# Kernel tuning notes

Hardware: AMD Instinct MI355X
Metric: run time of the kernel (lower is better)

The kernel has to match this reference:

```python
import jax, jax.numpy as jnp
import numpy as np

HEADS = 8
DIM_HEAD = 64
SCALE = DIM_HEAD ** -0.5
EPS = 1e-5


def layernorm(t, g, b):
    mu = t.mean(-1, keepdims=True)
    var = ((t - mu) ** 2).mean(-1, keepdims=True)
    return (t - mu) * jax.lax.rsqrt(var + EPS) * g + b


def setup_inputs() -> dict:
    key = jax.random.key(0)
    ks = jax.random.split(key, 12)
    b, n, dim, inner = 2, 2048, 512, HEADS * DIM_HEAD
    s = dim ** -0.5
    return {
        "x": jax.random.normal(ks[0], (b, n, dim), jnp.float32),
        "context": jax.random.normal(ks[1], (b, n, dim), jnp.float32),
        "g_x": jnp.ones((dim,), jnp.float32),
        "b_x": jnp.zeros((dim,), jnp.float32),
        "g_c": jnp.ones((dim,), jnp.float32),
        "b_c": jnp.zeros((dim,), jnp.float32),
        "W_qk": jax.random.normal(ks[2], (dim, inner), jnp.float32) * s,
        "W_cqk": jax.random.normal(ks[3], (dim, inner), jnp.float32) * s,
        "W_v": jax.random.normal(ks[4], (dim, inner), jnp.float32) * s,
        "W_cv": jax.random.normal(ks[5], (dim, inner), jnp.float32) * s,
        "W_out": jax.random.normal(ks[6], (inner, dim), jnp.float32) * s,
        "b_out": jnp.zeros((dim,), jnp.float32),
        "W_cout": jax.random.normal(ks[7], (inner, dim), jnp.float32) * s,
        "b_cout": jnp.zeros((dim,), jnp.float32),
    }


def reference(x, context, g_x, b_x, g_c, b_c, W_qk, W_cqk, W_v, W_cv, W_out, b_out, W_cout, b_cout):
    b, i, _ = x.shape
    j = context.shape[1]
    xn = layernorm(x, g_x, b_x)
    cn = layernorm(context, g_c, b_c)

    def split_heads(t):  # [b, n, h*d] -> [b, h, n, d]
        return t.reshape(t.shape[0], t.shape[1], HEADS, DIM_HEAD).transpose(0, 2, 1, 3)

    qk = split_heads(xn @ W_qk)
    cqk = split_heads(cn @ W_cqk)
    v = split_heads(xn @ W_v)
    cv = split_heads(cn @ W_cv)

    sim = jnp.einsum('bhid,bhjd->bhij', qk, cqk) * SCALE  # [b,h,i,j]
    attn = jax.nn.softmax(sim, axis=-1)           # rows: x attends to context
    context_attn = jax.nn.softmax(sim, axis=-2)   # cols: context attends to x

    out = jnp.einsum('bhij,bhjd->bhid', attn, cv)            # [b,h,i,d]
    context_out = jnp.einsum('bhij,bhid->bhjd', context_attn, v)  # [b,h,j,d]

    def merge_heads(t):  # [b,h,n,d] -> [b,n,h*d]
        return t.transpose(0, 2, 1, 3).reshape(t.shape[0], t.shape[2], HEADS * DIM_HEAD)

    out = merge_heads(out) @ W_out + b_out
    context_out = merge_heads(context_out) @ W_cout + b_cout
    return out, context_out
```

## Files before the change

### kernel.cpp

```cpp
#include <hip/hip_runtime.h>


typedef _Float16 half_t;
typedef __attribute__((ext_vector_type(2))) _Float16 half2v;
typedef __attribute__((ext_vector_type(4))) _Float16 half4v;
typedef __attribute__((ext_vector_type(8))) _Float16 half8v;
typedef __attribute__((ext_vector_type(4))) float floatx4;

#define MFMA16(a, b, c) __builtin_amdgcn_mfma_f32_16x16x32_f16((a), (b), (c), 0, 0, 0)

#if defined(__has_builtin)
#if __has_builtin(__builtin_amdgcn_exp2f)
#define EXP2F(x) __builtin_amdgcn_exp2f(x)
#else
#define EXP2F(x) exp2f(x)
#endif
#else
#define EXP2F(x) exp2f(x)
#endif

__device__ __forceinline__ half2v pk2(float a, float b) {
#if defined(__has_builtin) && __has_builtin(__builtin_amdgcn_cvt_pkrtz)
    union { __fp16 __attribute__((ext_vector_type(2))) i; half2v o; } u;
    u.i = __builtin_amdgcn_cvt_pkrtz(a, b);
    return u.o;
#else
    half2v r; r[0] = (half_t)a; r[1] = (half_t)b; return r;
#endif
}

__device__ __forceinline__ void gld16(const half_t* g, half_t* l) {
    __builtin_amdgcn_global_load_lds(
        (const __attribute__((address_space(1))) void*)g,
        (__attribute__((address_space(3))) void*)l, 16, 0, 0);
}

__global__ __launch_bounds__(256) void prep_kernel(
    const float* __restrict__ x, const float* __restrict__ ctx,
    const float* __restrict__ gx, const float* __restrict__ bx,
    const float* __restrict__ gc, const float* __restrict__ bc,
    half_t* __restrict__ xn, half_t* __restrict__ cn,
    const float* __restrict__ W0, const float* __restrict__ W1,
    const float* __restrict__ W2, const float* __restrict__ W3,
    const float* __restrict__ W4, const float* __restrict__ W5,
    half_t* __restrict__ Wt)
{
    __shared__ alignas(16) half_t Ts[128][136];
    const int blk = blockIdx.x;
    const int tid = threadIdx.x;
    const int wave = tid >> 6, lane = tid & 63;

    if (blk < 2048) {
        const int row = blk * 4 + wave;
        const float *src, *g, *b;
        half_t* dst;
        if (row < 4096) {
            src = x + (size_t)row * 512; g = gx; b = bx; dst = xn + (size_t)row * 512;
        } else {
            const size_t r = (size_t)(row - 4096);
            src = ctx + r * 512; g = gc; b = bc; dst = cn + r * 512;
        }
        const float4 a0 = *(const float4*)(src + lane * 4);
        const float4 a1 = *(const float4*)(src + 256 + lane * 4);
        float s = a0.x + a0.y + a0.z + a0.w + a1.x + a1.y + a1.z + a1.w;
        float q = a0.x * a0.x + a0.y * a0.y + a0.z * a0.z + a0.w * a0.w +
                  a1.x * a1.x + a1.y * a1.y + a1.z * a1.z + a1.w * a1.w;
#pragma unroll
        for (int m = 1; m < 64; m <<= 1) {
            s += __shfl_xor(s, m);
            q += __shfl_xor(q, m);
        }
        const float mean = s * (1.0f / 512.0f);
        const float var = q * (1.0f / 512.0f) - mean * mean;
        const float rs = rsqrtf(var + 1e-5f);
        const float4 g0 = *(const float4*)(g + lane * 4);
        const float4 g1 = *(const float4*)(g + 256 + lane * 4);
        const float4 b0 = *(const float4*)(b + lane * 4);
        const float4 b1 = *(const float4*)(b + 256 + lane * 4);
        half4v h0, h1;
        h0[0] = (half_t)((a0.x - mean) * rs * g0.x + b0.x);
        h0[1] = (half_t)((a0.y - mean) * rs * g0.y + b0.y);
        h0[2] = (half_t)((a0.z - mean) * rs * g0.z + b0.z);
        h0[3] = (half_t)((a0.w - mean) * rs * g0.w + b0.w);
        h1[0] = (half_t)((a1.x - mean) * rs * g1.x + b1.x);
        h1[1] = (half_t)((a1.y - mean) * rs * g1.y + b1.y);
        h1[2] = (half_t)((a1.z - mean) * rs * g1.z + b1.z);
        h1[3] = (half_t)((a1.w - mean) * rs * g1.w + b1.w);
        *(half4v*)(dst + lane * 4) = h0;
        *(half4v*)(dst + 256 + lane * 4) = h1;
        return;
    }

    const int b2 = blk - 2048;
    const int mat = b2 >> 4, tile = b2 & 15;
    const float* src;
    switch (mat) {
        case 0: src = W0; break;
        case 1: src = W1; break;
        case 2: src = W2; break;
        case 3: src = W3; break;
        case 4: src = W4; break;
        default: src = W5; break;
    }
    const int tr0 = (tile >> 2) * 128;
    const int tc0 = (tile & 3) * 128;
#pragma unroll
    for (int p = 0; p < 16; ++p) {
        const int idx = p * 256 + tid;
        const int r = idx >> 5, c4 = (idx & 31) * 4;
        const float4 w = *(const float4*)(src + (size_t)(tr0 + r) * 512 + tc0 + c4);
        Ts[c4 + 0][r] = (half_t)w.x;
        Ts[c4 + 1][r] = (half_t)w.y;
        Ts[c4 + 2][r] = (half_t)w.z;
        Ts[c4 + 3][r] = (half_t)w.w;
    }
    __syncthreads();
    half_t* dst = Wt + (size_t)mat * 262144;
#pragma unroll
    for (int p = 0; p < 8; ++p) {
        const int idx = p * 256 + tid;
        const int row = idx >> 4, ch = (idx & 15) * 8;
        *(half8v*)(dst + (size_t)(tc0 + row) * 512 + tr0 + ch) = *(const half8v*)&Ts[row][ch];
    }
}

__global__ __launch_bounds__(256) void gemm_in_kernel(
    const half_t* __restrict__ xn, const half_t* __restrict__ cn,
    const half_t* __restrict__ Wt,
    half_t* __restrict__ qk, half_t* __restrict__ v_t,
    half_t* __restrict__ cqk, half_t* __restrict__ cv_t)
{
    const half_t* A; const half_t* B; half_t* O;
    switch (blockIdx.z) {
        case 0:  A = xn; B = Wt;          O = qk;   break;
        case 1:  A = xn; B = Wt + 262144; O = v_t;  break;
        case 2:  A = cn; B = Wt + 524288; O = cqk;  break;
        default: A = cn; B = Wt + 786432; O = cv_t; break;
    }
    const int tr = blockIdx.z & 1;
    const int mt0 = blockIdx.x * 128;
    const int nt0 = blockIdx.y * 128;

    __shared__ alignas(16) half_t As[128 * 64];
    __shared__ alignas(16) half_t Ws[128 * 64];

    const int tid = threadIdx.x;
    const int wave = tid >> 6, lane = tid & 63;
    const int wr = wave >> 1, wc = wave & 1;
    const int q4 = lane >> 4, c = lane & 15;

    int srow[4], scol[4];
#pragma unroll
    for (int p = 0; p < 4; ++p) {
        const int ofs = p * 4096 + wave * 1024 + lane * 16;
        const int row = ofs >> 7;
        const int pc = (ofs >> 4) & 7;
        srow[p] = row;
        scol[p] = (pc ^ (row & 7)) * 8;
    }

    const half_t* P1 = tr ? As : Ws;
    const half_t* P2 = tr ? Ws : As;

    const floatx4 z4 = {0.f, 0.f, 0.f, 0.f};
    floatx4 acc[4][4];
#pragma unroll
    for (int mt = 0; mt < 4; ++mt)
#pragma unroll
        for (int nt = 0; nt < 4; ++nt) acc[mt][nt] = z4;

    for (int kb = 0; kb < 8; ++kb) {
        const int k0 = kb * 64;
#pragma unroll
        for (int p = 0; p < 4; ++p) {
            const int lofs = p * 2048 + wave * 512;
            gld16(A + (size_t)(mt0 + srow[p]) * 512 + k0 + scol[p], As + lofs);
            gld16(B + (size_t)(nt0 + srow[p]) * 512 + k0 + scol[p], Ws + lofs);
        }
        __syncthreads();
#pragma unroll
        for (int kt = 0; kt < 2; ++kt) {
            half8v f1[4], f2[4];
#pragma unroll
            for (int i = 0; i < 4; ++i) {
                const int r1 = wr * 64 + i * 16 + c;
                const int r2 = wc * 64 + i * 16 + c;
                f1[i] = *(const half8v*)&P1[(r1 << 6) + (((kt * 4 + q4) ^ (r1 & 7)) << 3)];
                f2[i] = *(const half8v*)&P2[(r2 << 6) + (((kt * 4 + q4) ^ (r2 & 7)) << 3)];
            }
#pragma unroll
            for (int mt = 0; mt < 4; ++mt)
#pragma unroll
                for (int nt = 0; nt < 4; ++nt)
                    acc[mt][nt] = MFMA16(f1[mt], f2[nt], acc[mt][nt]);
        }
        __syncthreads();
    }

    const int bb = mt0 >> 11;
    const int nnb = mt0 & 2047;
    if (tr) {
#pragma unroll
        for (int mt = 0; mt < 4; ++mt) {
            const int row = nnb + wr * 64 + mt * 16 + q4 * 4;
#pragma unroll
            for (int nt = 0; nt < 4; ++nt) {
                const int col = nt0 + wc * 64 + nt * 16 + c;
                const int h = col >> 6, dd = col & 63;
                half4v pk;
                pk[0] = (half_t)acc[mt][nt][0];
                pk[1] = (half_t)acc[mt][nt][1];
                pk[2] = (half_t)acc[mt][nt][2];
                pk[3] = (half_t)acc[mt][nt][3];
                *(half4v*)(O + ((size_t)(bb * 8 + h) * 64 + dd) * 2048 + row) = pk;
            }
        }
    } else {
#pragma unroll
        for (int mt = 0; mt < 4; ++mt) {
            const int colw = nt0 + wr * 64 + mt * 16 + q4 * 4;
            const int h = colw >> 6, dd = colw & 63;
#pragma unroll
            for (int nt = 0; nt < 4; ++nt) {
                const int row = nnb + wc * 64 + nt * 16 + c;
                half4v pk;
                pk[0] = (half_t)acc[mt][nt][0];
                pk[1] = (half_t)acc[mt][nt][1];
                pk[2] = (half_t)acc[mt][nt][2];
                pk[3] = (half_t)acc[mt][nt][3];
                *(half4v*)(O + ((size_t)(bb * 8 + h) * 2048 + row) * 64 + dd) = pk;
            }
        }
    }
}

__global__ __launch_bounds__(256, 2) void flash_kernel(
    const half_t* __restrict__ qk, const half_t* __restrict__ cqk,
    const half_t* __restrict__ v_t, const half_t* __restrict__ cv_t,
    half_t* __restrict__ out_h, half_t* __restrict__ ctx_out_h)
{
    const int bh = blockIdx.x, it = blockIdx.y, dir = blockIdx.z;
    const half_t* Q  = dir ? cqk : qk;
    const half_t* K  = dir ? qk  : cqk;
    const half_t* VT = dir ? v_t : cv_t;
    half_t* Out = dir ? ctx_out_h : out_h;
    const half_t* Qb = Q + (size_t)bh * (2048 * 64);
    const half_t* Kb = K + (size_t)bh * (2048 * 64);
    const half_t* VTb = VT + (size_t)bh * (64 * 2048);

    __shared__ alignas(16) half_t Ks[128 * 64];
    __shared__ alignas(16) half_t CVs[64 * 128];

    const int tid = threadIdx.x;
    const int wave = tid >> 6, lane = tid & 63;
    const int q4 = lane >> 4, c = lane & 15;

    half8v onesb;
#pragma unroll
    for (int j = 0; j < 8; ++j) onesb[j] = (c == 0) ? (half_t)1.0f : (half_t)0.0f;

    half8v qf[2][2];
#pragma unroll
    for (int mt = 0; mt < 2; ++mt)
#pragma unroll
        for (int kt = 0; kt < 2; ++kt) {
            half8v v = *(const half8v*)(Qb + (size_t)(it * 128 + wave * 32 + mt * 16 + c) * 64 +
                                        kt * 32 + q4 * 8);
            qf[mt][kt] = v * (half_t)0.18033688f;
        }

    const floatx4 z4 = {0.f, 0.f, 0.f, 0.f};
    floatx4 accT[4][2];
    floatx4 accL[2];
#pragma unroll
    for (int vt = 0; vt < 4; ++vt)
#pragma unroll
        for (int mt = 0; mt < 2; ++mt) accT[vt][mt] = z4;
    accL[0] = z4; accL[1] = z4;

    half8v kpre[4], vpre[4];
#pragma unroll
    for (int p = 0; p < 4; ++p) {
        const int cidx = p * 256 + tid;
        kpre[p] = *(const half8v*)(Kb + (size_t)(cidx >> 3) * 64 + (cidx & 7) * 8);
        vpre[p] = *(const half8v*)(VTb + (size_t)(cidx >> 4) * 2048 + (cidx & 15) * 8);
    }

    for (int jt = 0; jt < 16; ++jt) {
        __syncthreads();
#pragma unroll
        for (int p = 0; p < 4; ++p) {
            const int cidx = p * 256 + tid;
            const int krow = cidx >> 3, kch = cidx & 7;
            *(half8v*)&Ks[krow * 64 + ((kch ^ ((krow >> 2) & 7)) * 8)] = kpre[p];
            const int vrow = cidx >> 4, vch = cidx & 15;
            *(half8v*)&CVs[vrow * 128 + ((vch ^ (vrow & 15)) * 8)] = vpre[p];
        }
        __syncthreads();
        if (jt < 15) {
            const half_t* Kt = Kb + (size_t)(jt + 1) * 8192;
            const half_t* Vt = VTb + (jt + 1) * 128;
#pragma unroll
            for (int p = 0; p < 4; ++p) {
                const int cidx = p * 256 + tid;
                kpre[p] = *(const half8v*)(Kt + (size_t)(cidx >> 3) * 64 + (cidx & 7) * 8);
                vpre[p] = *(const half8v*)(Vt + (size_t)(cidx >> 4) * 2048 + (cidx & 15) * 8);
            }
        }

#pragma unroll
        for (int g = 0; g < 4; ++g) {
            floatx4 st[2][2];
#pragma unroll
            for (int t = 0; t < 2; ++t) {
                const int jr = g * 32 + t * 4 + ((c >> 2) << 3) + (c & 3);
                const int sw = (jr >> 2) & 7;
                const half8v kf0 = *(const half8v*)&Ks[jr * 64 + ((q4 ^ sw) * 8)];
                const half8v kf1 = *(const half8v*)&Ks[jr * 64 + (((4 + q4) ^ sw) * 8)];
#pragma unroll
                for (int mt = 0; mt < 2; ++mt) {
                    floatx4 tt = MFMA16(kf0, qf[mt][0], z4);
                    st[mt][t] = MFMA16(kf1, qf[mt][1], tt);
                }
            }
            half8v pf[2];
#pragma unroll
            for (int mt = 0; mt < 2; ++mt) {
                union { half8v v; half2v h2[4]; } u;
                u.h2[0] = pk2(EXP2F(fminf(st[mt][0][0], 15.0f)),
                              EXP2F(fminf(st[mt][0][1], 15.0f)));
                u.h2[1] = pk2(EXP2F(fminf(st[mt][0][2], 15.0f)),
                              EXP2F(fminf(st[mt][0][3], 15.0f)));
                u.h2[2] = pk2(EXP2F(fminf(st[mt][1][0], 15.0f)),
                              EXP2F(fminf(st[mt][1][1], 15.0f)));
                u.h2[3] = pk2(EXP2F(fminf(st[mt][1][2], 15.0f)),
                              EXP2F(fminf(st[mt][1][3], 15.0f)));
                pf[mt] = u.v;
            }
#pragma unroll
            for (int vt = 0; vt < 4; ++vt) {
                const half8v bf = *(const half8v*)&CVs[(vt * 16 + c) * 128 +
                                                       (((g * 4 + q4) ^ c) * 8)];
#pragma unroll
                for (int mt = 0; mt < 2; ++mt)
                    accT[vt][mt] = MFMA16(bf, pf[mt], accT[vt][mt]);
            }
#pragma unroll
            for (int mt = 0; mt < 2; ++mt)
                accL[mt] = MFMA16(onesb, pf[mt], accL[mt]);
        }
    }

    const size_t ob = (size_t)(bh >> 3) * 2048 * 512 + (size_t)(bh & 7) * 64;
#pragma unroll
    for (int mt = 0; mt < 2; ++mt) {
        const float l = __shfl(accL[mt][0], c);
        const float rl = 1.0f / l;
        const int row = it * 128 + wave * 32 + mt * 16 + c;
#pragma unroll
        for (int vt = 0; vt < 4; ++vt) {
            half4v pk;
            pk[0] = (half_t)(accT[vt][mt][0] * rl);
            pk[1] = (half_t)(accT[vt][mt][1] * rl);
            pk[2] = (half_t)(accT[vt][mt][2] * rl);
            pk[3] = (half_t)(accT[vt][mt][3] * rl);
            *(half4v*)(Out + ob + (size_t)row * 512 + vt * 16 + q4 * 4) = pk;
        }
    }
}

__global__ __launch_bounds__(256) void gemm_out_kernel(
    const half_t* __restrict__ out_h, const half_t* __restrict__ ctx_out_h,
    const half_t* __restrict__ Wt,
    const float* __restrict__ bout, const float* __restrict__ bcout,
    float* __restrict__ dout)
{
    const half_t* A; const half_t* B; const float* bias; float* O;
    if (blockIdx.z == 0) { A = out_h;     B = Wt + 1048576; bias = bout;  O = dout; }
    else                 { A = ctx_out_h; B = Wt + 1310720; bias = bcout; O = dout + 2097152; }

    const int mt0 = blockIdx.x * 64;
    const int nt0 = blockIdx.y * 128;

    __shared__ alignas(16) half_t As[64 * 64];
    __shared__ alignas(16) half_t Ws[128 * 64];

    const int tid = threadIdx.x;
    const int wave = tid >> 6, lane = tid & 63;
    const int wr = wave >> 1, wc = wave & 1;
    const int q4 = lane >> 4, c = lane & 15;

    int srow[4], scol[4];
#pragma unroll
    for (int p = 0; p < 4; ++p) {
        const int ofs = p * 4096 + wave * 1024 + lane * 16;
        const int row = ofs >> 7;
        const int pc = (ofs >> 4) & 7;
        srow[p] = row;
        scol[p] = (pc ^ (row & 7)) * 8;
    }

    const floatx4 z4 = {0.f, 0.f, 0.f, 0.f};
    floatx4 acc[4][2];
#pragma unroll
    for (int mt = 0; mt < 4; ++mt)
#pragma unroll
        for (int nt = 0; nt < 2; ++nt) acc[mt][nt] = z4;

    for (int kb = 0; kb < 8; ++kb) {
        const int k0 = kb * 64;
#pragma unroll
        for (int p = 0; p < 4; ++p) {
            const int lofs = p * 2048 + wave * 512;
            gld16(B + (size_t)(nt0 + srow[p]) * 512 + k0 + scol[p], Ws + lofs);
            if (p < 2)
                gld16(A + (size_t)(mt0 + srow[p]) * 512 + k0 + scol[p], As + lofs);
        }
        __syncthreads();
#pragma unroll
        for (int kt = 0; kt < 2; ++kt) {
            half8v f1[4], f2[2];
#pragma unroll
            for (int i = 0; i < 4; ++i) {
                const int r1 = wr * 64 + i * 16 + c;
                f1[i] = *(const half8v*)&Ws[(r1 << 6) + (((kt * 4 + q4) ^ (r1 & 7)) << 3)];
            }
#pragma unroll
            for (int i = 0; i < 2; ++i) {
                const int r2 = wc * 32 + i * 16 + c;
                f2[i] = *(const half8v*)&As[(r2 << 6) + (((kt * 4 + q4) ^ (r2 & 7)) << 3)];
            }
#pragma unroll
            for (int mt = 0; mt < 4; ++mt)
#pragma unroll
                for (int nt = 0; nt < 2; ++nt)
                    acc[mt][nt] = MFMA16(f1[mt], f2[nt], acc[mt][nt]);
        }
        __syncthreads();
    }

#pragma unroll
    for (int mt = 0; mt < 4; ++mt) {
        const int col = nt0 + wr * 64 + mt * 16 + q4 * 4;
        const float4 bv = *(const float4*)(bias + col);
#pragma unroll
        for (int nt = 0; nt < 2; ++nt) {
            const int row = mt0 + wc * 32 + nt * 16 + c;
            float4 o;
            o.x = acc[mt][nt][0] + bv.x;
            o.y = acc[mt][nt][1] + bv.y;
            o.z = acc[mt][nt][2] + bv.z;
            o.w = acc[mt][nt][3] + bv.w;
            *(float4*)(O + (size_t)row * 512 + col) = o;
        }
    }
}

extern "C" void kernel_launch(void* const* d_in, const int* in_sizes, int n_in,
                              void* d_out, int out_size, void* d_ws, size_t ws_size,
                              hipStream_t stream)
{
    (void)in_sizes; (void)n_in; (void)out_size; (void)ws_size;
    const float* x      = (const float*)d_in[0];
    const float* ctx    = (const float*)d_in[1];
    const float* g_x    = (const float*)d_in[2];
    const float* b_x    = (const float*)d_in[3];
    const float* g_c    = (const float*)d_in[4];
    const float* b_c    = (const float*)d_in[5];
    const float* W_qk   = (const float*)d_in[6];
    const float* W_cqk  = (const float*)d_in[7];
    const float* W_v    = (const float*)d_in[8];
    const float* W_cv   = (const float*)d_in[9];
    const float* W_out  = (const float*)d_in[10];
    const float* b_out  = (const float*)d_in[11];
    const float* W_cout = (const float*)d_in[12];
    const float* b_cout = (const float*)d_in[13];
    float* out = (float*)d_out;

    half_t* ws = (half_t*)d_ws;
    const size_t SEG = 2097152;
    half_t* xn        = ws;
    half_t* cn        = ws + 1 * SEG;
    half_t* qk        = ws + 2 * SEG;
    half_t* cqk       = ws + 3 * SEG;
    half_t* v_t       = ws + 4 * SEG;
    half_t* cv_t      = ws + 5 * SEG;
    half_t* Wt        = ws + 6 * SEG;
    half_t* out_h     = xn;
    half_t* ctx_out_h = cn;

    prep_kernel<<<2144, 256, 0, stream>>>(x, ctx, g_x, b_x, g_c, b_c, xn, cn,
                                          W_qk, W_v, W_cqk, W_cv, W_out, W_cout, Wt);
    gemm_in_kernel<<<dim3(32, 4, 4), 256, 0, stream>>>(xn, cn, Wt, qk, v_t, cqk, cv_t);
    flash_kernel<<<dim3(16, 16, 2), 256, 0, stream>>>(qk, cqk, v_t, cv_t, out_h, ctx_out_h);
    gemm_out_kernel<<<dim3(64, 4, 2), 256, 0, stream>>>(out_h, ctx_out_h, Wt, b_out, b_cout, out);
}
```

Before: 171.7 us.

## Double-buffer LDS tiles with async global-to-LDS loads in all kernels

Adds double-buffered shared-memory tiles to the input GEMM, flash attention and output GEMM kernels, so the next K-tile is issued into the alternate buffer while the current one is consumed. This drops one barrier per iteration. In the flash kernel it also replaces the register-staged prefetch with direct global-to-LDS loads (gld16), writing swizzled addresses from the global side. The cost is doubled LDS use, which can lower occupancy, particularly for the flash kernel with launch_bounds(256,2). The single barrier also depends on gld16 completing before __syncthreads.

```diff
diff --git a/kernel.cpp b/kernel.cpp
--- a/kernel.cpp
+++ b/kernel.cpp
@@ -141,8 +141,8 @@
     const int mt0 = blockIdx.x * 128;
     const int nt0 = blockIdx.y * 128;
 
-    __shared__ alignas(16) half_t As[128 * 64];
-    __shared__ alignas(16) half_t Ws[128 * 64];
+    __shared__ alignas(16) half_t As[2][128 * 64];
+    __shared__ alignas(16) half_t Ws[2][128 * 64];
 
     const int tid = threadIdx.x;
     const int wave = tid >> 6, lane = tid & 63;
@@ -159,9 +159,6 @@
         scol[p] = (pc ^ (row & 7)) * 8;
     }
 
-    const half_t* P1 = tr ? As : Ws;
-    const half_t* P2 = tr ? Ws : As;
-
     const floatx4 z4 = {0.f, 0.f, 0.f, 0.f};
     floatx4 acc[4][4];
 #pragma unroll
@@ -169,15 +166,22 @@
 #pragma unroll
         for (int nt = 0; nt < 4; ++nt) acc[mt][nt] = z4;
 
-    for (int kb = 0; kb < 8; ++kb) {
+    auto stage = [&](int kb, int buf) {
         const int k0 = kb * 64;
 #pragma unroll
         for (int p = 0; p < 4; ++p) {
             const int lofs = p * 2048 + wave * 512;
-            gld16(A + (size_t)(mt0 + srow[p]) * 512 + k0 + scol[p], As + lofs);
-            gld16(B + (size_t)(nt0 + srow[p]) * 512 + k0 + scol[p], Ws + lofs);
-        }
+            gld16(A + (size_t)(mt0 + srow[p]) * 512 + k0 + scol[p], &As[buf][lofs]);
+            gld16(B + (size_t)(nt0 + srow[p]) * 512 + k0 + scol[p], &Ws[buf][lofs]);
+        }
+    };
+
+    stage(0, 0);
+    for (int kb = 0; kb < 8; ++kb) {
         __syncthreads();
+        if (kb < 7) stage(kb + 1, (kb + 1) & 1);
+        const half_t* P1 = tr ? As[kb & 1] : Ws[kb & 1];
+        const half_t* P2 = tr ? Ws[kb & 1] : As[kb & 1];
 #pragma unroll
         for (int kt = 0; kt < 2; ++kt) {
             half8v f1[4], f2[4];
@@ -194,7 +198,6 @@
                 for (int nt = 0; nt < 4; ++nt)
                     acc[mt][nt] = MFMA16(f1[mt], f2[nt], acc[mt][nt]);
         }
-        __syncthreads();
     }
 
     const int bb = mt0 >> 11;
@@ -248,8 +251,8 @@
     const half_t* Kb = K + (size_t)bh * (2048 * 64);
     const half_t* VTb = VT + (size_t)bh * (64 * 2048);
 
-    __shared__ alignas(16) half_t Ks[128 * 64];
-    __shared__ alignas(16) half_t CVs[64 * 128];
+    __shared__ alignas(16) half_t Ks[2][128 * 64];
+    __shared__ alignas(16) half_t CVs[2][64 * 128];
 
     const int tid = threadIdx.x;
     const int wave = tid >> 6, lane = tid & 63;
@@ -278,35 +281,27 @@
         for (int mt = 0; mt < 2; ++mt) accT[vt][mt] = z4;
     accL[0] = z4; accL[1] = z4;
 
-    half8v kpre[4], vpre[4];
-#pragma unroll
-    for (int p = 0; p < 4; ++p) {
-        const int cidx = p * 256 + tid;
-        kpre[p] = *(const half8v*)(Kb + (size_t)(cidx >> 3) * 64 + (cidx & 7) * 8);
-        vpre[p] = *(const half8v*)(VTb + (size_t)(cidx >> 4) * 2048 + (cidx & 15) * 8);
-    }
-
-    for (int jt = 0; jt < 16; ++jt) {
-        __syncthreads();
+    auto stage = [&](int jt, int buf) {
+        const half_t* Kt = Kb + (size_t)jt * 8192;
+        const half_t* Vt = VTb + jt * 128;
 #pragma unroll
         for (int p = 0; p < 4; ++p) {
             const int cidx = p * 256 + tid;
             const int krow = cidx >> 3, kch = cidx & 7;
-            *(half8v*)&Ks[krow * 64 + ((kch ^ ((krow >> 2) & 7)) * 8)] = kpre[p];
+            gld16(Kt + krow * 64 + ((kch ^ ((krow >> 2) & 7)) * 8),
+                  &Ks[buf][(p * 256 + wave * 64) * 8]);
             const int vrow = cidx >> 4, vch = cidx & 15;
-            *(half8v*)&CVs[vrow * 128 + ((vch ^ (vrow & 15)) * 8)] = vpre[p];
-        }
+            gld16(Vt + (size_t)vrow * 2048 + ((vch ^ (vrow & 15)) * 8),
+                  &CVs[buf][(p * 256 + wave * 64) * 8]);
+        }
+    };
+
+    stage(0, 0);
+    for (int jt = 0; jt < 16; ++jt) {
         __syncthreads();
-        if (jt < 15) {
-            const half_t* Kt = Kb + (size_t)(jt + 1) * 8192;
-            const half_t* Vt = VTb + (jt + 1) * 128;
-#pragma unroll
-            for (int p = 0; p < 4; ++p) {
-                const int cidx = p * 256 + tid;
-                kpre[p] = *(const half8v*)(Kt + (size_t)(cidx >> 3) * 64 + (cidx & 7) * 8);
-                vpre[p] = *(const half8v*)(Vt + (size_t)(cidx >> 4) * 2048 + (cidx & 15) * 8);
-            }
-        }
+        if (jt < 15) stage(jt + 1, (jt + 1) & 1);
+        const half_t* Ksb = Ks[jt & 1];
+        const half_t* CVsb = CVs[jt & 1];
 
 #pragma unroll
         for (int g = 0; g < 4; ++g) {
@@ -315,8 +310,8 @@
             for (int t = 0; t < 2; ++t) {
                 const int jr = g * 32 + t * 4 + ((c >> 2) << 3) + (c & 3);
                 const int sw = (jr >> 2) & 7;
-                const half8v kf0 = *(const half8v*)&Ks[jr * 64 + ((q4 ^ sw) * 8)];
-                const half8v kf1 = *(const half8v*)&Ks[jr * 64 + (((4 + q4) ^ sw) * 8)];
+                const half8v kf0 = *(const half8v*)&Ksb[jr * 64 + ((q4 ^ sw) * 8)];
+                const half8v kf1 = *(const half8v*)&Ksb[jr * 64 + (((4 + q4) ^ sw) * 8)];
 #pragma unroll
                 for (int mt = 0; mt < 2; ++mt) {
                     floatx4 tt = MFMA16(kf0, qf[mt][0], z4);
@@ -339,8 +334,8 @@
             }
 #pragma unroll
             for (int vt = 0; vt < 4; ++vt) {
-                const half8v bf = *(const half8v*)&CVs[(vt * 16 + c) * 128 +
-                                                       (((g * 4 + q4) ^ c) * 8)];
+                const half8v bf = *(const half8v*)&CVsb[(vt * 16 + c) * 128 +
+                                                        (((g * 4 + q4) ^ c) * 8)];
 #pragma unroll
                 for (int mt = 0; mt < 2; ++mt)
                     accT[vt][mt] = MFMA16(bf, pf[mt], accT[vt][mt]);
@@ -382,8 +377,8 @@
     const int mt0 = blockIdx.x * 64;
     const int nt0 = blockIdx.y * 128;
 
-    __shared__ alignas(16) half_t As[64 * 64];
-    __shared__ alignas(16) half_t Ws[128 * 64];
+    __shared__ alignas(16) half_t As[2][64 * 64];
+    __shared__ alignas(16) half_t Ws[2][128 * 64];
 
     const int tid = threadIdx.x;
     const int wave = tid >> 6, lane = tid & 63;
@@ -407,28 +402,35 @@
 #pragma unroll
         for (int nt = 0; nt < 2; ++nt) acc[mt][nt] = z4;
 
-    for (int kb = 0; kb < 8; ++kb) {
+    auto stage = [&](int kb, int buf) {
         const int k0 = kb * 64;
 #pragma unroll
         for (int p = 0; p < 4; ++p) {
             const int lofs = p * 2048 + wave * 512;
-            gld16(B + (size_t)(nt0 + srow[p]) * 512 + k0 + scol[p], Ws + lofs);
+            gld16(B + (size_t)(nt0 + srow[p]) * 512 + k0 + scol[p], &Ws[buf][lofs]);
             if (p < 2)
-                gld16(A + (size_t)(mt0 + srow[p]) * 512 + k0 + scol[p], As + lofs);
-        }
+                gld16(A + (size_t)(mt0 + srow[p]) * 512 + k0 + scol[p], &As[buf][lofs]);
+        }
+    };
+
+    stage(0, 0);
+    for (int kb = 0; kb < 8; ++kb) {
         __syncthreads();
+        if (kb < 7) stage(kb + 1, (kb + 1) & 1);
+        const half_t* Ab = As[kb & 1];
+        const half_t* Wb = Ws[kb & 1];
 #pragma unroll
         for (int kt = 0; kt < 2; ++kt) {
             half8v f1[4], f2[2];
 #pragma unroll
             for (int i = 0; i < 4; ++i) {
                 const int r1 = wr * 64 + i * 16 + c;
-                f1[i] = *(const half8v*)&Ws[(r1 << 6) + (((kt * 4 + q4) ^ (r1 & 7)) << 3)];
+                f1[i] = *(const half8v*)&Wb[(r1 << 6) + (((kt * 4 + q4) ^ (r1 & 7)) << 3)];
             }
 #pragma unroll
             for (int i = 0; i < 2; ++i) {
                 const int r2 = wc * 32 + i * 16 + c;
-                f2[i] = *(const half8v*)&As[(r2 << 6) + (((kt * 4 + q4) ^ (r2 & 7)) << 3)];
+                f2[i] = *(const half8v*)&Ab[(r2 << 6) + (((kt * 4 + q4) ^ (r2 & 7)) << 3)];
             }
 #pragma unroll
             for (int mt = 0; mt < 4; ++mt)
@@ -436,7 +438,6 @@
                 for (int nt = 0; nt < 2; ++nt)
                     acc[mt][nt] = MFMA16(f1[mt], f2[nt], acc[mt][nt]);
         }
-        __syncthreads();
     }
 
 #pragma unroll
```

After: 172.4 us. Within noise of the previous version (+0.4%).
